# Performance work log

Measured on AMD Instinct MI355X. Metric: run time of the kernel, lower is better.

## Reference

```python
import jax, jax.numpy as jnp
import numpy as np

B, L, D = 8, 4096, 1024
EPS = 1e-6


def setup_inputs() -> dict:
    key = jax.random.key(0)
    k1, k2, k3 = jax.random.split(key, 3)
    x = jax.random.normal(k1, (B, L, D), dtype=jnp.float32)
    # torch.nn.Linear default init ~ U(-1/sqrt(d), 1/sqrt(d)); scaled normal is fine for a reference
    w_in = jax.random.normal(k2, (3 * D, D), dtype=jnp.float32) * (D ** -0.5)
    w_out = jax.random.normal(k3, (D, D), dtype=jnp.float32) * (D ** -0.5)
    scale = jnp.ones((D,), dtype=jnp.float32)
    return {"x": x, "w_in": w_in, "w_out": w_out, "scale": scale}


def reference(x, w_in, w_out, scale):
    residual = x
    # RMSNorm: ||x||_2 * d^{-1/2}
    norm = jnp.linalg.norm(x, axis=-1, keepdims=True) * (x.shape[-1] ** -0.5)
    xn = scale * x / (norm + EPS)
    # proj_in: Linear(d, 3d, bias=False) -> chunk into g, v, f
    gvf = jnp.einsum('bld,ed->ble', xn, w_in)  # [B, L, 3D]
    g, v, f = jnp.split(gvf, 3, axis=-1)
    g = jax.nn.sigmoid(g)
    f = jax.nn.sigmoid(f - 1.0)

    # sequential gated linear recurrence: h_t = f_t * h_{t-1} + (1 - f_t) * v_t
    def step(h, fv):
        ft, vt = fv  # each [B, D]
        h = ft * h + (1.0 - ft) * vt
        return h, h

    h0 = jnp.zeros((x.shape[0], x.shape[2]), dtype=x.dtype)
    _, h_seq = jax.lax.scan(step, h0, (jnp.swapaxes(f, 0, 1), jnp.swapaxes(v, 0, 1)))
    h_seq = jnp.swapaxes(h_seq, 0, 1)  # [B, L, D]

    out = g * h_seq
    return residual + jnp.einsum('bld,ed->ble', out, w_out)
```

## Files before the change

### kernel.cpp

```cpp
#include <hip/hip_runtime.h>
#include <cstdint>
#include <cstddef>

typedef unsigned short u16;
typedef __attribute__((ext_vector_type(8))) short short8;
typedef __attribute__((ext_vector_type(4))) float floatx4;
typedef __attribute__((ext_vector_type(4))) unsigned short ushort4v;

constexpr int D_ = 1024;
constexpr int B_ = 8;
constexpr int L_ = 4096;
constexpr int M_ = B_ * L_;
constexpr int NCHUNK = 64;
constexpr int CLEN = L_ / NCHUNK;
constexpr float EPS_ = 1e-6f;
constexpr size_t WIN_ELEMS = (size_t)3 * D_ * D_;
constexpr size_t WOUT_ELEMS = (size_t)D_ * D_;
constexpr int NT_K = 16;
constexpr int PREPW_BLOCKS = (int)((WIN_ELEMS + WOUT_ELEMS) / 8 / 256);

__device__ __forceinline__ float bf2f(u16 b) {
    union { unsigned u; float f; } x; x.u = ((unsigned)b) << 16; return x.f;
}
__device__ __forceinline__ u16 f2bf(float f) {
    union { float f; unsigned u; } x; x.f = f;
    unsigned r = x.u + 0x7fffu + ((x.u >> 16) & 1u);
    return (u16)(r >> 16);
}
__device__ __forceinline__ float sigmoidf_(float x) {
    return 1.f / (1.f + __expf(-x));
}
__device__ __forceinline__ short8 cvt8(const float* __restrict__ p) {
    float4 a = *(const float4*)p;
    float4 b = *(const float4*)(p + 4);
    short8 o;
    o[0] = (short)f2bf(a.x); o[1] = (short)f2bf(a.y);
    o[2] = (short)f2bf(a.z); o[3] = (short)f2bf(a.w);
    o[4] = (short)f2bf(b.x); o[5] = (short)f2bf(b.y);
    o[6] = (short)f2bf(b.z); o[7] = (short)f2bf(b.w);
    return o;
}
__device__ __forceinline__ void gload16(const void* g, void* l) {
    __builtin_amdgcn_global_load_lds((const __attribute__((address_space(1))) void*)g,
                                     (__attribute__((address_space(3))) void*)l, 16, 0, 0);
}

__global__ __launch_bounds__(256) void prep_kernel(const float* __restrict__ x,
                                                   const float* __restrict__ scale,
                                                   u16* __restrict__ xn,
                                                   const float* __restrict__ w_in,
                                                   const float* __restrict__ w_out,
                                                   u16* __restrict__ w_in_bf,
                                                   u16* __restrict__ w_out_bf) {
    const int t = threadIdx.x;
    if ((int)blockIdx.x >= M_) {
        size_t i8 = ((size_t)(blockIdx.x - M_) * 256 + t) * 8;
        if (i8 < WIN_ELEMS) {
            *(short8*)(w_in_bf + i8) = cvt8(w_in + i8);
        } else {
            size_t j = i8 - WIN_ELEMS;
            *(short8*)(w_out_bf + j) = cvt8(w_out + j);
        }
        return;
    }
    const int row = blockIdx.x;
    const float* xr = x + (size_t)row * D_;
    float4 xv = ((const float4*)xr)[t];
    float ss = xv.x * xv.x + xv.y * xv.y + xv.z * xv.z + xv.w * xv.w;
#pragma unroll
    for (int m = 32; m >= 1; m >>= 1) ss += __shfl_xor(ss, m, 64);
    __shared__ float red[4];
    const int wave = t >> 6, lane = t & 63;
    if (lane == 0) red[wave] = ss;
    __syncthreads();
    float tot = red[0] + red[1] + red[2] + red[3];
    float inv = 1.f / (sqrtf(tot * (1.f / D_)) + EPS_);
    float4 sv = ((const float4*)scale)[t];
    ushort4v o;
    o[0] = f2bf(xv.x * inv * sv.x);
    o[1] = f2bf(xv.y * inv * sv.y);
    o[2] = f2bf(xv.z * inv * sv.z);
    o[3] = f2bf(xv.w * inv * sv.w);
    ((ushort4v*)(xn + (size_t)row * D_))[t] = o;
}


#define STAGE_A_(buf, half, koff) do { \
    const u16* g_ = gA0 + (koff) + (half) * 65536; \
    u16* l_ = (buf) + ((half) * 64 + iw) * 64; \
    gload16(g_, l_); gload16(g_ + 131072, l_ + 8192); } while (0)
#define STAGE_B_(buf, half, koff) do { \
    const u16* g_ = gB0 + (koff) + (half) * 32768; \
    u16* l_ = (buf) + (rBw + (half) * 32) * 64; \
    gload16(g_, l_); gload16(g_ + 131072, l_ + 8192); } while (0)
#define BARRIER_() do { __builtin_amdgcn_sched_barrier(0); \
    __builtin_amdgcn_s_barrier(); \
    __builtin_amdgcn_sched_barrier(0); } while (0)
#define LDA4_(mlo) do { \
    _Pragma("unroll") for (int m_ = 0; m_ < 4; ++m_) { \
      int o_ = aOff + ((mlo) + m_) * 2048; \
      af[m_][0] = *(const short8*)((const char*)curA + o_); \
      af[m_][1] = *(const short8*)((const char*)curA + (o_ ^ 64)); } } while (0)
#define LDB2_(nlo) do { \
    _Pragma("unroll") for (int n_ = 0; n_ < 2; ++n_) { \
      int o_ = bOff + ((nlo) + n_) * 2048; \
      bfv[(nlo) + n_][0] = *(const short8*)((const char*)curB + o_); \
      bfv[(nlo) + n_][1] = *(const short8*)((const char*)curB + (o_ ^ 64)); } } while (0)
#define MFMA_Q_(mlo, nlo) do { \
    __builtin_amdgcn_s_setprio(1); \
    _Pragma("unroll") for (int m_ = 0; m_ < 4; ++m_) \
    _Pragma("unroll") for (int n_ = 0; n_ < 2; ++n_) \
    _Pragma("unroll") for (int k_ = 0; k_ < 2; ++k_) \
      acc[(mlo) + m_][(nlo) + n_] = __builtin_amdgcn_mfma_f32_16x16x32_bf16( \
          af[m_][k_], bfv[(nlo) + n_][k_], acc[(mlo) + m_][(nlo) + n_], 0, 0, 0); \
    __builtin_amdgcn_s_setprio(0); } while (0)

__device__ __forceinline__ void tile_step(int tt, u16* curA, u16* curB, u16* othA, u16* othB,
                                          const u16* gA0, const u16* gB0, int iw, int rBw,
                                          int aOff, int bOff, floatx4 (&acc)[8][4]) {
    short8 af[4][2], bfv[4][2];
    const int k1 = (tt + 1) * 64, k2 = (tt + 2) * 64;
    const bool s1 = (tt + 1 < NT_K), s2 = (tt + 2 < NT_K);
    LDA4_(0); LDB2_(0);
    if (s1) STAGE_A_(othA, 1, k1);
    MFMA_Q_(0, 0);
    BARRIER_();
    LDB2_(2);
    if (s1) STAGE_B_(othB, 1, k1);
    MFMA_Q_(0, 2);
    BARRIER_();
    LDA4_(4);
    if (s2) STAGE_A_(curA, 0, k2);
    MFMA_Q_(4, 0);
    BARRIER_();
    if (s2) STAGE_B_(curB, 0, k2);
    MFMA_Q_(4, 2);
    if (s2)      { asm volatile("s_waitcnt vmcnt(4)" ::: "memory"); }
    else if (s1) { asm volatile("s_waitcnt vmcnt(0)" ::: "memory"); }
    BARRIER_();
}

__device__ __forceinline__ void gemm256_core(const u16* __restrict__ gA,
                                             const u16* __restrict__ gB,
                                             int m0, int n0,
                                             u16* __restrict__ As, u16* __restrict__ Bs,
                                             floatx4 (&acc)[8][4]) {
    const int t = threadIdx.x;
    const int wid = t >> 6, lane = t & 63;
    const int wr = wid >> 2, wc = wid & 3;
    const int l15 = lane & 15, quad = lane >> 4;
    const int jrow = lane >> 3, jc = lane & 7;
    const int swz = ((jc ^ (jrow & 7)) << 3);
    const u16* gA0 = gA + (size_t)(m0 + wid * 8 + jrow) * 1024 + swz;
    const int i0 = wid * 8 + jrow;
    const int rB0 = ((i0 >> 5) << 6) + (i0 & 31);
    const u16* gB0 = gB + (size_t)(n0 + rB0) * 1024 + swz;
    const int iw = wid * 8;
    const int rBw = ((iw >> 5) << 6) + (iw & 31);
    const int c0 = (quad * 16) ^ ((l15 & 7) << 4);
    const int aOff = (wr * 128 + l15) * 128 + c0;
    const int bOff = (wc * 64 + l15) * 128 + c0;

#pragma unroll
    for (int i = 0; i < 8; i++)
#pragma unroll
        for (int j = 0; j < 4; j++) { floatx4 z = {0.f, 0.f, 0.f, 0.f}; acc[i][j] = z; }

    STAGE_A_(As, 0, 0); STAGE_A_(As, 1, 0);
    STAGE_B_(Bs, 0, 0); STAGE_B_(Bs, 1, 0);
    STAGE_A_(As + 16384, 0, 64);
    STAGE_B_(Bs + 16384, 0, 64);
    asm volatile("s_waitcnt vmcnt(4)" ::: "memory");
    BARRIER_();

#pragma unroll 1
    for (int tt = 0; tt < NT_K; tt += 2) {
        tile_step(tt,     As,         Bs,         As + 16384, Bs + 16384,
                  gA0, gB0, iw, rBw, aOff, bOff, acc);
        tile_step(tt + 1, As + 16384, Bs + 16384, As,         Bs,
                  gA0, gB0, iw, rBw, aOff, bOff, acc);
    }
}

__global__ __launch_bounds__(512, 2) void gemm1_kernel(const u16* __restrict__ xn,
                                                       const u16* __restrict__ w_in,
                                                       u16* __restrict__ g_buf,
                                                       u16* __restrict__ v_buf,
                                                       u16* __restrict__ f_buf) {
    __shared__ __align__(16) u16 SH[65536];
    const int m0 = blockIdx.y * 256;
    const int n0 = blockIdx.x * 256;
    floatx4 acc[8][4];
    gemm256_core(xn, w_in, m0, n0, SH, SH + 32768, acc);

    const int t = threadIdx.x;
    const int wid = t >> 6, lane = t & 63;
    const int wr = wid >> 2, wc = wid & 3;
    const int l15 = lane & 15, quad = lane >> 4;
    const int plane = n0 >> 10;
    const int cbase = n0 & 1023;
    u16* dst = (plane == 0) ? g_buf : ((plane == 1) ? v_buf : f_buf);

#pragma unroll
    for (int mt = 0; mt < 8; mt++) {
#pragma unroll
        for (int r = 0; r < 4; r++) {
            int row = wr * 128 + mt * 16 + quad * 4 + r;
            int xr = (row & 7) << 3;
#pragma unroll
            for (int nt = 0; nt < 4; nt++) {
                int colb = (wc * 64 + nt * 16 + l15) * 2;
                float val = acc[mt][nt][r];
                if (plane == 0) val = sigmoidf_(val);
                else if (plane == 2) val = sigmoidf_(val - 1.f);
                *(u16*)((char*)SH + row * 512 + (colb ^ xr)) = f2bf(val);
            }
        }
    }
    __syncthreads();
    const int lane8 = lane * 8;
#pragma unroll 4
    for (int i = 0; i < 32; i++) {
        int row = wid + i * 8;
        int xr = (row & 7) << 3;
        uint2 v = *(const uint2*)((const char*)SH + row * 512 + (lane8 ^ xr));
        *(uint2*)(dst + (size_t)(m0 + row) * 1024 + cbase + lane * 4) = v;
    }
}

__global__ __launch_bounds__(512, 2) void gemm2_kernel(const u16* __restrict__ op,
                                                       const u16* __restrict__ w_out,
                                                       const float* __restrict__ xres,
                                                       float* __restrict__ out) {
    __shared__ __align__(16) u16 SH[65536];
    const int m0 = blockIdx.y * 256;
    const int n0 = blockIdx.x * 256;
    floatx4 acc[8][4];
    gemm256_core(op, w_out, m0, n0, SH, SH + 32768, acc);

    const int t = threadIdx.x;
    const int wid = t >> 6, lane = t & 63;
    const int wr = wid >> 2, wc = wid & 3;
    const int l15 = lane & 15, quad = lane >> 4;
    const int ncol0 = n0 + wc * 64;
    const int mrow0 = m0 + wr * 128 + quad * 4;
#pragma unroll
    for (int mt = 0; mt < 8; mt++) {
#pragma unroll
        for (int r = 0; r < 4; r++) {
            int m = mrow0 + mt * 16 + r;
#pragma unroll
            for (int nt = 0; nt < 4; nt++) {
                size_t idx = (size_t)m * 1024 + ncol0 + nt * 16 + l15;
                out[idx] = acc[mt][nt][r] + xres[idx];
            }
        }
    }
}

__global__ __launch_bounds__(256) void scan1_kernel(const u16* __restrict__ f_buf,
                                                    const u16* __restrict__ v_buf,
                                                    float* __restrict__ Aarr,
                                                    float* __restrict__ Barr) {
    const int wid = blockIdx.x * 4 + (threadIdx.x >> 6);
    const int lane = threadIdx.x & 63;
    const int b = wid >> 10;
    const int rem = wid & 1023;
    const int c = rem >> 4;
    const int db = (rem & 15) * 64 + lane;
    float A = 1.f, Bv = 0.f;
    size_t base = ((size_t)b * L_ + c * CLEN) * D_ + db;
#pragma unroll 4
    for (int tt = 0; tt < CLEN; tt++) {
        float fv = bf2f(f_buf[base + (size_t)tt * D_]);
        float vv = bf2f(v_buf[base + (size_t)tt * D_]);
        A *= fv;
        Bv = fv * Bv + (1.f - fv) * vv;
    }
    size_t sidx = ((size_t)b * NCHUNK + c) * D_ + db;
    Aarr[sidx] = A;
    Barr[sidx] = Bv;
}

__global__ __launch_bounds__(256) void scan2_kernel(const float* __restrict__ Aarr,
                                                    const float* __restrict__ Barr,
                                                    float* __restrict__ hin) {
    const int id = blockIdx.x * 256 + threadIdx.x;
    const int b = id >> 10, d = id & 1023;
    float h = 0.f;
    for (int c = 0; c < NCHUNK; c++) {
        size_t idx = ((size_t)b * NCHUNK + c) * D_ + d;
        hin[idx] = h;
        h = Aarr[idx] * h + Barr[idx];
    }
}

__global__ __launch_bounds__(256) void scan3_kernel(const u16* __restrict__ f_buf,
                                                    const u16* __restrict__ v_buf,
                                                    u16* g_io,
                                                    const float* __restrict__ hin) {
    const int wid = blockIdx.x * 4 + (threadIdx.x >> 6);
    const int lane = threadIdx.x & 63;
    const int b = wid >> 10;
    const int rem = wid & 1023;
    const int c = rem >> 4;
    const int db = (rem & 15) * 64 + lane;
    size_t base = ((size_t)b * L_ + c * CLEN) * D_ + db;
    float h = hin[((size_t)b * NCHUNK + c) * D_ + db];
#pragma unroll 4
    for (int tt = 0; tt < CLEN; tt++) {
        size_t idx = base + (size_t)tt * D_;
        float fv = bf2f(f_buf[idx]);
        float vv = bf2f(v_buf[idx]);
        float gv = bf2f(g_io[idx]);
        h = fv * h + (1.f - fv) * vv;
        g_io[idx] = f2bf(gv * h);
    }
}

extern "C" void kernel_launch(void* const* d_in, const int* in_sizes, int n_in,
                              void* d_out, int out_size, void* d_ws, size_t ws_size,
                              hipStream_t stream) {
    const float* x     = (const float*)d_in[0];
    const float* w_in  = (const float*)d_in[1];
    const float* w_out = (const float*)d_in[2];
    const float* scale = (const float*)d_in[3];
    float* out = (float*)d_out;

    u16* f_buf = (u16*)d_out;
    u16* v_buf = (u16*)d_out + (size_t)M_ * D_;

    char* ws = (char*)d_ws;
    const size_t PLANE = (size_t)M_ * D_ * sizeof(u16);
    u16* xn    = (u16*)ws;
    u16* g_buf = (u16*)(ws + PLANE);
    u16* w_in_bf  = (u16*)(ws + 2 * PLANE);
    u16* w_out_bf = w_in_bf + WIN_ELEMS;
    float* Aarr = (float*)(ws + 2 * PLANE + (WIN_ELEMS + WOUT_ELEMS) * sizeof(u16));
    float* Barr = Aarr + (size_t)B_ * NCHUNK * D_;
    float* hin  = Barr + (size_t)B_ * NCHUNK * D_;

    prep_kernel<<<M_ + PREPW_BLOCKS, 256, 0, stream>>>(x, scale, xn, w_in, w_out,
                                                       w_in_bf, w_out_bf);
    gemm1_kernel<<<dim3(3 * D_ / 256, M_ / 256), 512, 0, stream>>>(
        xn, w_in_bf, g_buf, v_buf, f_buf);
    scan1_kernel<<<(B_ * NCHUNK * 16) / 4, 256, 0, stream>>>(f_buf, v_buf, Aarr, Barr);
    scan2_kernel<<<(B_ * D_) / 256, 256, 0, stream>>>(Aarr, Barr, hin);
    scan3_kernel<<<(B_ * NCHUNK * 16) / 4, 256, 0, stream>>>(f_buf, v_buf, g_buf, hin);
    gemm2_kernel<<<dim3(D_ / 256, M_ / 256), 512, 0, stream>>>(g_buf, w_out_bf, x, out);
}
```

Baseline: 617.5 us.

## Restructure GEMM core into four-stage K=32 LDS ring with register double-buffering

Replaces the two-buffer K=64 tile pipeline, which used XOR-swizzled LDS and quartered MFMA phases, with a four-slot ring of K=32 slices. Each step reads the whole fragment set into alternating register sets (s0/s1) while the next slice is being staged from global memory. The goal is to hide LDS read latency behind MFMAs and to cut barriers and address math per MFMA. In exchange it drops the swizzle, so LDS bank conflicts may rise, and the extra fragment registers raise register pressure at 2 blocks per CU.

```diff
diff --git a/kernel.cpp b/kernel.cpp
--- a/kernel.cpp
+++ b/kernel.cpp
@@ -16,7 +16,6 @@
 constexpr float EPS_ = 1e-6f;
 constexpr size_t WIN_ELEMS = (size_t)3 * D_ * D_;
 constexpr size_t WOUT_ELEMS = (size_t)D_ * D_;
-constexpr int NT_K = 16;
 constexpr int PREPW_BLOCKS = (int)((WIN_ELEMS + WOUT_ELEMS) / 8 / 256);
 
 __device__ __forceinline__ float bf2f(u16 b) {
@@ -85,101 +84,79 @@
 }
 
 
-#define STAGE_A_(buf, half, koff) do { \
-    const u16* g_ = gA0 + (koff) + (half) * 65536; \
-    u16* l_ = (buf) + ((half) * 64 + iw) * 64; \
-    gload16(g_, l_); gload16(g_ + 131072, l_ + 8192); } while (0)
-#define STAGE_B_(buf, half, koff) do { \
-    const u16* g_ = gB0 + (koff) + (half) * 32768; \
-    u16* l_ = (buf) + (rBw + (half) * 32) * 64; \
-    gload16(g_, l_); gload16(g_ + 131072, l_ + 8192); } while (0)
 #define BARRIER_() do { __builtin_amdgcn_sched_barrier(0); \
     __builtin_amdgcn_s_barrier(); \
     __builtin_amdgcn_sched_barrier(0); } while (0)
-#define LDA4_(mlo) do { \
-    _Pragma("unroll") for (int m_ = 0; m_ < 4; ++m_) { \
-      int o_ = aOff + ((mlo) + m_) * 2048; \
-      af[m_][0] = *(const short8*)((const char*)curA + o_); \
-      af[m_][1] = *(const short8*)((const char*)curA + (o_ ^ 64)); } } while (0)
-#define LDB2_(nlo) do { \
-    _Pragma("unroll") for (int n_ = 0; n_ < 2; ++n_) { \
-      int o_ = bOff + ((nlo) + n_) * 2048; \
-      bfv[(nlo) + n_][0] = *(const short8*)((const char*)curB + o_); \
-      bfv[(nlo) + n_][1] = *(const short8*)((const char*)curB + (o_ ^ 64)); } } while (0)
-#define MFMA_Q_(mlo, nlo) do { \
-    __builtin_amdgcn_s_setprio(1); \
-    _Pragma("unroll") for (int m_ = 0; m_ < 4; ++m_) \
-    _Pragma("unroll") for (int n_ = 0; n_ < 2; ++n_) \
-    _Pragma("unroll") for (int k_ = 0; k_ < 2; ++k_) \
-      acc[(mlo) + m_][(nlo) + n_] = __builtin_amdgcn_mfma_f32_16x16x32_bf16( \
-          af[m_][k_], bfv[(nlo) + n_][k_], acc[(mlo) + m_][(nlo) + n_], 0, 0, 0); \
+#define VM4_() asm volatile("s_waitcnt vmcnt(4)" ::: "memory")
+#define VM0_() asm volatile("s_waitcnt vmcnt(0)" ::: "memory")
+
+#define RD_(S, bsel) do { \
+    const char* aP_ = ((bsel) < 2 ? aLo : aHi) + ((bsel) & 1) * 32768; \
+    const char* bP_ = ((bsel) < 2 ? bLo : bHi) + ((bsel) & 1) * 32768; \
+    _Pragma("unroll") for (int m_ = 0; m_ < 8; ++m_) \
+        S##a[m_] = *(const short8*)(aP_ + m_ * 1024); \
+    _Pragma("unroll") for (int n_ = 0; n_ < 4; ++n_) \
+        S##b[n_] = *(const short8*)(bP_ + n_ * 1024); \
+} while (0)
+
+#define STAGE_(bsel, pa, pb, koff) do { \
+    u16* lA_ = SH + (bsel) * 16384 + wid * 512; \
+    gload16((pa) + (koff), lA_);            gload16((pa) + (koff) + 131072, lA_ + 4096); \
+    gload16((pb) + (koff), lA_ + 8192);     gload16((pb) + (koff) + 131072, lA_ + 12288); \
+} while (0)
+
+#define MFMA_(S) do { __builtin_amdgcn_s_setprio(1); \
+    _Pragma("unroll") for (int m_ = 0; m_ < 8; ++m_) \
+    _Pragma("unroll") for (int n_ = 0; n_ < 4; ++n_) \
+        acc[m_][n_] = __builtin_amdgcn_mfma_f32_16x16x32_bf16( \
+            S##a[m_], S##b[n_], acc[m_][n_], 0, 0, 0); \
     __builtin_amdgcn_s_setprio(0); } while (0)
-
-__device__ __forceinline__ void tile_step(int tt, u16* curA, u16* curB, u16* othA, u16* othB,
-                                          const u16* gA0, const u16* gB0, int iw, int rBw,
-                                          int aOff, int bOff, floatx4 (&acc)[8][4]) {
-    short8 af[4][2], bfv[4][2];
-    const int k1 = (tt + 1) * 64, k2 = (tt + 2) * 64;
-    const bool s1 = (tt + 1 < NT_K), s2 = (tt + 2 < NT_K);
-    LDA4_(0); LDB2_(0);
-    if (s1) STAGE_A_(othA, 1, k1);
-    MFMA_Q_(0, 0);
-    BARRIER_();
-    LDB2_(2);
-    if (s1) STAGE_B_(othB, 1, k1);
-    MFMA_Q_(0, 2);
-    BARRIER_();
-    LDA4_(4);
-    if (s2) STAGE_A_(curA, 0, k2);
-    MFMA_Q_(4, 0);
-    BARRIER_();
-    if (s2) STAGE_B_(curB, 0, k2);
-    MFMA_Q_(4, 2);
-    if (s2)      { asm volatile("s_waitcnt vmcnt(4)" ::: "memory"); }
-    else if (s1) { asm volatile("s_waitcnt vmcnt(0)" ::: "memory"); }
-    BARRIER_();
-}
 
 __device__ __forceinline__ void gemm256_core(const u16* __restrict__ gA,
                                              const u16* __restrict__ gB,
                                              int m0, int n0,
-                                             u16* __restrict__ As, u16* __restrict__ Bs,
+                                             u16* __restrict__ SH,
                                              floatx4 (&acc)[8][4]) {
     const int t = threadIdx.x;
     const int wid = t >> 6, lane = t & 63;
     const int wr = wid >> 2, wc = wid & 3;
     const int l15 = lane & 15, quad = lane >> 4;
-    const int jrow = lane >> 3, jc = lane & 7;
-    const int swz = ((jc ^ (jrow & 7)) << 3);
-    const u16* gA0 = gA + (size_t)(m0 + wid * 8 + jrow) * 1024 + swz;
-    const int i0 = wid * 8 + jrow;
-    const int rB0 = ((i0 >> 5) << 6) + (i0 & 31);
-    const u16* gB0 = gB + (size_t)(n0 + rB0) * 1024 + swz;
-    const int iw = wid * 8;
-    const int rBw = ((iw >> 5) << 6) + (iw & 31);
-    const int c0 = (quad * 16) ^ ((l15 & 7) << 4);
-    const int aOff = (wr * 128 + l15) * 128 + c0;
-    const int bOff = (wc * 64 + l15) * 128 + c0;
-
+
+    const u16* gA0 = gA + (size_t)(m0 + (t >> 2)) * 1024 + (t & 3) * 8;
+    const u16* gB0 = gB + (size_t)(n0 + (t >> 2)) * 1024 + (t & 3) * 8;
+    char* aLo = (char*)SH + (wr * 128 + l15) * 64 + quad * 16;
+    char* aHi = aLo + 65536;
+    char* bLo = (char*)SH + 16384 + (wc * 64 + l15) * 64 + quad * 16;
+    char* bHi = bLo + 65536;
+
+    short8 s0a[8], s0b[4], s1a[8], s1b[4];
 #pragma unroll
     for (int i = 0; i < 8; i++)
 #pragma unroll
         for (int j = 0; j < 4; j++) { floatx4 z = {0.f, 0.f, 0.f, 0.f}; acc[i][j] = z; }
 
-    STAGE_A_(As, 0, 0); STAGE_A_(As, 1, 0);
-    STAGE_B_(Bs, 0, 0); STAGE_B_(Bs, 1, 0);
-    STAGE_A_(As + 16384, 0, 64);
-    STAGE_B_(Bs + 16384, 0, 64);
-    asm volatile("s_waitcnt vmcnt(4)" ::: "memory");
+    STAGE_(0, gA0, gB0, 0);
+    STAGE_(1, gA0, gB0, 32);
+    STAGE_(2, gA0, gB0, 64);
+    VM4_();
     BARRIER_();
-
+    RD_(s0, 0);
+
+    const u16* gAs = gA0 + 96;
+    const u16* gBs = gB0 + 96;
 #pragma unroll 1
-    for (int tt = 0; tt < NT_K; tt += 2) {
-        tile_step(tt,     As,         Bs,         As + 16384, Bs + 16384,
-                  gA0, gB0, iw, rBw, aOff, bOff, acc);
-        tile_step(tt + 1, As + 16384, Bs + 16384, As,         Bs,
-                  gA0, gB0, iw, rBw, aOff, bOff, acc);
-    }
+    for (int it = 0; it < 7; ++it) {
+        RD_(s1, 1); STAGE_(3, gAs, gBs, 0);  MFMA_(s0); VM4_(); BARRIER_();
+        RD_(s0, 2); STAGE_(0, gAs, gBs, 32); MFMA_(s1); VM4_(); BARRIER_();
+        RD_(s1, 3); STAGE_(1, gAs, gBs, 64); MFMA_(s0); VM4_(); BARRIER_();
+        RD_(s0, 0); STAGE_(2, gAs, gBs, 96); MFMA_(s1); VM4_(); BARRIER_();
+        gAs += 128; gBs += 128;
+    }
+    RD_(s1, 1); STAGE_(3, gAs, gBs, 0); MFMA_(s0); VM4_(); BARRIER_();
+    RD_(s0, 2);                         MFMA_(s1); VM0_(); BARRIER_();
+    RD_(s1, 3);                         MFMA_(s0);
+    MFMA_(s1);
+    BARRIER_();
 }
 
 __global__ __launch_bounds__(512, 2) void gemm1_kernel(const u16* __restrict__ xn,
@@ -191,7 +168,7 @@
     const int m0 = blockIdx.y * 256;
     const int n0 = blockIdx.x * 256;
     floatx4 acc[8][4];
-    gemm256_core(xn, w_in, m0, n0, SH, SH + 32768, acc);
+    gemm256_core(xn, w_in, m0, n0, SH, acc);
 
     const int t = threadIdx.x;
     const int wid = t >> 6, lane = t & 63;
@@ -236,7 +213,7 @@
     const int m0 = blockIdx.y * 256;
     const int n0 = blockIdx.x * 256;
     floatx4 acc[8][4];
-    gemm256_core(op, w_out, m0, n0, SH, SH + 32768, acc);
+    gemm256_core(op, w_out, m0, n0, SH, acc);
 
     const int t = threadIdx.x;
     const int wid = t >> 6, lane = t & 63;
```

Result: slower. 721.2 us (+16.8%).

## Vectorize scan kernels to 4 channels per thread and trim GEMM barriers

Applied to the files above, without the earlier changes.

The three scan kernels now give each thread four adjacent channels and use 8-byte bf16 and 16-byte float vector loads and stores. This cuts the number of memory instructions and improves access width, but launches 4x fewer threads. scan2 in particular drops to 8 blocks, which lowers parallelism for its latency-bound loop. Separately, the GEMM tile step now issues the LDS reads and the next-stage A and B staging together, dropping two barriers per k-step; this risks a race if staging overwrites buffers other waves are still reading.

```diff
diff --git a/kernel.cpp b/kernel.cpp
--- a/kernel.cpp
+++ b/kernel.cpp
@@ -121,19 +121,14 @@
     short8 af[4][2], bfv[4][2];
     const int k1 = (tt + 1) * 64, k2 = (tt + 2) * 64;
     const bool s1 = (tt + 1 < NT_K), s2 = (tt + 2 < NT_K);
-    LDA4_(0); LDB2_(0);
-    if (s1) STAGE_A_(othA, 1, k1);
+    LDA4_(0); LDB2_(0); LDB2_(2);
+    if (s1) { STAGE_A_(othA, 1, k1); STAGE_B_(othB, 1, k1); }
     MFMA_Q_(0, 0);
-    BARRIER_();
-    LDB2_(2);
-    if (s1) STAGE_B_(othB, 1, k1);
     MFMA_Q_(0, 2);
     BARRIER_();
     LDA4_(4);
-    if (s2) STAGE_A_(curA, 0, k2);
+    if (s2) { STAGE_A_(curA, 0, k2); STAGE_B_(curB, 0, k2); }
     MFMA_Q_(4, 0);
-    BARRIER_();
-    if (s2) STAGE_B_(curB, 0, k2);
     MFMA_Q_(4, 2);
     if (s2)      { asm volatile("s_waitcnt vmcnt(4)" ::: "memory"); }
     else if (s1) { asm volatile("s_waitcnt vmcnt(0)" ::: "memory"); }
@@ -264,34 +259,47 @@
                                                     float* __restrict__ Barr) {
     const int wid = blockIdx.x * 4 + (threadIdx.x >> 6);
     const int lane = threadIdx.x & 63;
-    const int b = wid >> 10;
-    const int rem = wid & 1023;
-    const int c = rem >> 4;
-    const int db = (rem & 15) * 64 + lane;
-    float A = 1.f, Bv = 0.f;
-    size_t base = ((size_t)b * L_ + c * CLEN) * D_ + db;
-#pragma unroll 4
+    const int b = wid >> 8;
+    const int rem = wid & 255;
+    const int c = rem >> 2;
+    const int d0 = (rem & 3) * 256 + lane * 4;
+    float A[4], Bv[4];
+#pragma unroll
+    for (int j = 0; j < 4; j++) { A[j] = 1.f; Bv[j] = 0.f; }
+    size_t base = ((size_t)b * L_ + c * CLEN) * D_ + d0;
+#pragma unroll 2
     for (int tt = 0; tt < CLEN; tt++) {
-        float fv = bf2f(f_buf[base + (size_t)tt * D_]);
-        float vv = bf2f(v_buf[base + (size_t)tt * D_]);
-        A *= fv;
-        Bv = fv * Bv + (1.f - fv) * vv;
-    }
-    size_t sidx = ((size_t)b * NCHUNK + c) * D_ + db;
-    Aarr[sidx] = A;
-    Barr[sidx] = Bv;
+        ushort4v f4 = *(const ushort4v*)(f_buf + base + (size_t)tt * D_);
+        ushort4v v4 = *(const ushort4v*)(v_buf + base + (size_t)tt * D_);
+#pragma unroll
+        for (int j = 0; j < 4; j++) {
+            float fv = bf2f(f4[j]);
+            float vv = bf2f(v4[j]);
+            A[j] *= fv;
+            Bv[j] = fv * Bv[j] + (1.f - fv) * vv;
+        }
+    }
+    size_t sidx = ((size_t)b * NCHUNK + c) * D_ + d0;
+    floatx4 oA = {A[0], A[1], A[2], A[3]};
+    floatx4 oB = {Bv[0], Bv[1], Bv[2], Bv[3]};
+    *(floatx4*)(Aarr + sidx) = oA;
+    *(floatx4*)(Barr + sidx) = oB;
 }
 
 __global__ __launch_bounds__(256) void scan2_kernel(const float* __restrict__ Aarr,
                                                     const float* __restrict__ Barr,
                                                     float* __restrict__ hin) {
     const int id = blockIdx.x * 256 + threadIdx.x;
-    const int b = id >> 10, d = id & 1023;
-    float h = 0.f;
+    const int b = id >> 8, d0 = (id & 255) * 4;
+    float h[4] = {0.f, 0.f, 0.f, 0.f};
     for (int c = 0; c < NCHUNK; c++) {
-        size_t idx = ((size_t)b * NCHUNK + c) * D_ + d;
-        hin[idx] = h;
-        h = Aarr[idx] * h + Barr[idx];
+        size_t idx = ((size_t)b * NCHUNK + c) * D_ + d0;
+        floatx4 oh = {h[0], h[1], h[2], h[3]};
+        *(floatx4*)(hin + idx) = oh;
+        floatx4 a = *(const floatx4*)(Aarr + idx);
+        floatx4 bb = *(const floatx4*)(Barr + idx);
+#pragma unroll
+        for (int j = 0; j < 4; j++) h[j] = a[j] * h[j] + bb[j];
     }
 }
 
@@ -301,20 +309,29 @@
                                                     const float* __restrict__ hin) {
     const int wid = blockIdx.x * 4 + (threadIdx.x >> 6);
     const int lane = threadIdx.x & 63;
-    const int b = wid >> 10;
-    const int rem = wid & 1023;
-    const int c = rem >> 4;
-    const int db = (rem & 15) * 64 + lane;
-    size_t base = ((size_t)b * L_ + c * CLEN) * D_ + db;
-    float h = hin[((size_t)b * NCHUNK + c) * D_ + db];
-#pragma unroll 4
+    const int b = wid >> 8;
+    const int rem = wid & 255;
+    const int c = rem >> 2;
+    const int d0 = (rem & 3) * 256 + lane * 4;
+    size_t base = ((size_t)b * L_ + c * CLEN) * D_ + d0;
+    floatx4 hv = *(const floatx4*)(hin + ((size_t)b * NCHUNK + c) * D_ + d0);
+    float h[4] = {hv[0], hv[1], hv[2], hv[3]};
+#pragma unroll 2
     for (int tt = 0; tt < CLEN; tt++) {
         size_t idx = base + (size_t)tt * D_;
-        float fv = bf2f(f_buf[idx]);
-        float vv = bf2f(v_buf[idx]);
-        float gv = bf2f(g_io[idx]);
-        h = fv * h + (1.f - fv) * vv;
-        g_io[idx] = f2bf(gv * h);
+        ushort4v f4 = *(const ushort4v*)(f_buf + idx);
+        ushort4v v4 = *(const ushort4v*)(v_buf + idx);
+        ushort4v g4 = *(const ushort4v*)(g_io + idx);
+        ushort4v o;
+#pragma unroll
+        for (int j = 0; j < 4; j++) {
+            float fv = bf2f(f4[j]);
+            float vv = bf2f(v4[j]);
+            float gv = bf2f(g4[j]);
+            h[j] = fv * h[j] + (1.f - fv) * vv;
+            o[j] = f2bf(gv * h[j]);
+        }
+        *(ushort4v*)(g_io + idx) = o;
     }
 }
 
@@ -344,8 +361,8 @@
                                                        w_in_bf, w_out_bf);
     gemm1_kernel<<<dim3(3 * D_ / 256, M_ / 256), 512, 0, stream>>>(
         xn, w_in_bf, g_buf, v_buf, f_buf);
-    scan1_kernel<<<(B_ * NCHUNK * 16) / 4, 256, 0, stream>>>(f_buf, v_buf, Aarr, Barr);
-    scan2_kernel<<<(B_ * D_) / 256, 256, 0, stream>>>(Aarr, Barr, hin);
-    scan3_kernel<<<(B_ * NCHUNK * 16) / 4, 256, 0, stream>>>(f_buf, v_buf, g_buf, hin);
+    scan1_kernel<<<512, 256, 0, stream>>>(f_buf, v_buf, Aarr, Barr);
+    scan2_kernel<<<8, 256, 0, stream>>>(Aarr, Barr, hin);
+    scan3_kernel<<<512, 256, 0, stream>>>(f_buf, v_buf, g_buf, hin);
     gemm2_kernel<<<dim3(D_ / 256, M_ / 256), 512, 0, stream>>>(g_buf, w_out_bf, x, out);
 }
```

After: 614.9 us. About the same (-0.4%).
